# Kernel tuning notes

Measured on AMD Instinct MI355X. Metric: run time of the kernel, lower is better.

The kernel has to match this reference:

```python
import jax, jax.numpy as jnp
import numpy as np

T = 8
TAU = 2.0
V_TH = 1.0
V_RESET = 0.0
ALPHA = 2.0  # ATan surrogate alpha

@jax.custom_vjp
def spike(v):
    # Heaviside(v) with ATan surrogate gradient
    return (v >= 0.0).astype(v.dtype)

def _spike_fwd(v):
    return spike(v), v

def _spike_bwd(v, g):
    sg = (ALPHA / 2.0) / (1.0 + (jnp.pi / 2.0 * ALPHA * v) ** 2)
    return (g * sg,)

spike.defvjp(_spike_fwd, _spike_bwd)

def conv2d(x, w):
    return jax.lax.conv_general_dilated(x, w, (1, 1), 'SAME',
                                        dimension_numbers=('NCHW', 'OIHW', 'NCHW'))

def batchnorm(x, g, b, m, v):
    # inference-mode BN over channel dim of NCHW
    scale = (g / jnp.sqrt(v + 1e-5))[None, :, None, None]
    return (x - m[None, :, None, None]) * scale + b[None, :, None, None]

def maxpool2(x):
    return jax.lax.reduce_window(x, -jnp.inf, jax.lax.max,
                                 (1, 1, 2, 2), (1, 1, 2, 2), 'VALID')

def if_scan(x_seq):
    # x_seq: [T, ...]; IF neuron: v += x; spike; hard reset
    def step(v, x_t):
        v = v + x_t
        s = spike(v - V_TH)
        v = v * (1.0 - s) + V_RESET * s
        return v, s
    v0 = jnp.full_like(x_seq[0], V_RESET)
    _, s_seq = jax.lax.scan(step, v0, x_seq)
    return s_seq

def lif_scan(x_seq):
    # LIF neuron: v += (x - (v - v_reset)) / tau; spike; hard reset
    def step(v, x_t):
        v = v + (x_t - (v - V_RESET)) / TAU
        s = spike(v - V_TH)
        v = v * (1.0 - s) + V_RESET * s
        return v, s
    v0 = jnp.full_like(x_seq[0], V_RESET)
    _, s_seq = jax.lax.scan(step, v0, x_seq)
    return s_seq

def setup_inputs() -> dict:
    key = jax.random.key(0)
    ks = jax.random.split(key, 6)
    B = 64
    d = {
        'x': jax.random.normal(ks[0], (B, 1, 28, 28), dtype=jnp.float32),
        'conv1_w': jax.random.normal(ks[1], (128, 1, 3, 3), dtype=jnp.float32) * 0.3,
        'bn1_g': jnp.ones((128,), jnp.float32),
        'bn1_b': jnp.zeros((128,), jnp.float32),
        'bn1_m': jnp.zeros((128,), jnp.float32),
        'bn1_v': jnp.ones((128,), jnp.float32),
        'conv2_w': jax.random.normal(ks[2], (128, 128, 3, 3), dtype=jnp.float32) * 0.05,
        'bn2_g': jnp.ones((128,), jnp.float32),
        'bn2_b': jnp.zeros((128,), jnp.float32),
        'bn2_m': jnp.zeros((128,), jnp.float32),
        'bn2_v': jnp.ones((128,), jnp.float32),
        'fc1_w': jax.random.normal(ks[3], (128 * 3 * 3, 128 * 7 * 7), dtype=jnp.float32) * 0.02,
        'fc2_w': jax.random.normal(ks[4], (128, 128 * 3 * 3), dtype=jnp.float32) * 0.05,
        'fc3_w': jax.random.normal(ks[5], (10, 128), dtype=jnp.float32) * 0.1,
    }
    return d

def reference(x, conv1_w, bn1_g, bn1_b, bn1_m, bn1_v,
              conv2_w, bn2_g, bn2_b, bn2_m, bn2_v,
              fc1_w, fc2_w, fc3_w):
    B = x.shape[0]
    # static conv + BN (applied once, repeated T times)
    y0 = batchnorm(conv2d(x, conv1_w), bn1_g, bn1_b, bn1_m, bn1_v)  # [B,128,28,28]
    x_seq = jnp.broadcast_to(y0, (T,) + y0.shape)
    s1 = if_scan(x_seq)  # [T,B,128,28,28]
    # pool -> conv -> BN per timestep (vectorized over T*B)
    h = s1.reshape((T * B, 128, 28, 28))
    h = maxpool2(h)                       # [TB,128,14,14]
    h = batchnorm(conv2d(h, conv2_w), bn2_g, bn2_b, bn2_m, bn2_v)
    s2 = if_scan(h.reshape((T, B, 128, 14, 14)))
    # pool -> flatten (dropout is identity in eval mode)
    h = maxpool2(s2.reshape((T * B, 128, 14, 14)))  # [TB,128,7,7]
    h = h.reshape((T, B, 128 * 7 * 7))
    h = jnp.einsum('tbi,oi->tbo', h, fc1_w)   # [T,B,1152]
    s3 = lif_scan(h)
    h = jnp.einsum('tbi,oi->tbo', s3, fc2_w)  # [T,B,128]
    s4 = lif_scan(h)
    h = jnp.einsum('tbi,oi->tbo', s4, fc3_w)  # [T,B,10]
    s5 = lif_scan(h)
    return s5.sum(0) / T
```

## Files before the change

### kernel.cpp

```cpp
#include <hip/hip_runtime.h>
#include <hip/hip_bf16.h>
#include <cstddef>


typedef __attribute__((ext_vector_type(8))) short  short8;
typedef __attribute__((ext_vector_type(4))) float  f32x4;
typedef __attribute__((ext_vector_type(8))) __bf16 bf16x8;

__device__ inline short f2bf_bits(float x) {
    __hip_bfloat16 h = __float2bfloat16(x);
    return *reinterpret_cast<short*>(&h);
}
__device__ inline float bfbits2f(short b) {
    __hip_bfloat16 h;
    *reinterpret_cast<short*>(&h) = b;
    return __bfloat162float(h);
}

__global__ __launch_bounds__(256) void prep2_kernel(
    const float* __restrict__ w2, const float* __restrict__ g2,
    const float* __restrict__ v2, __hip_bfloat16* __restrict__ w2s,
    float* __restrict__ sc2)
{
    int id = blockIdx.x * 256 + threadIdx.x;
    if (id < 128) sc2[id] = g2[id] / sqrtf(v2[id] + 1e-5f);
    int ci = id & 127;
    int co = (id >> 7) & 127;
    int k  = id >> 14;
    float w  = w2[(co * 128 + ci) * 9 + k];
    float hi = __bfloat162float(__float2bfloat16(w));
    float r1 = w - hi;
    float md = __bfloat162float(__float2bfloat16(r1));
    float r2 = r1 - md;
    size_t base = ((size_t)k * 128 + co) * 128 + ci;
    const size_t SPL = 9 * 128 * 128;
    w2s[0 * SPL + base] = __float2bfloat16(hi);
    w2s[1 * SPL + base] = __float2bfloat16(md);
    w2s[2 * SPL + base] = __float2bfloat16(r2);
}

__global__ __launch_bounds__(256) void prep_fc1_kernel(
    const float* __restrict__ w, short* __restrict__ w1s)
{
    int id = blockIdx.x * 256 + threadIdx.x;
    int koct = id % 784;
    int n    = id / 784;
    const float* src = w + (size_t)n * 6272 + koct * 8;
    float4 va = *(const float4*)src;
    float4 vb = *(const float4*)(src + 4);
    float wv[8] = {va.x, va.y, va.z, va.w, vb.x, vb.y, vb.z, vb.w};
    short8 hi8, md8, lo8;
#pragma unroll
    for (int e = 0; e < 8; ++e) {
        float x  = wv[e];
        short hb = f2bf_bits(x);
        float r1 = x - bfbits2f(hb);
        short mb = f2bf_bits(r1);
        float r2 = r1 - bfbits2f(mb);
        hi8[e] = hb; md8[e] = mb; lo8[e] = f2bf_bits(r2);
    }
    const size_t SPL = (size_t)1152 * 6272;
    size_t base = (size_t)n * 6272 + koct * 8;
    *(short8*)&w1s[0 * SPL + base] = hi8;
    *(short8*)&w1s[1 * SPL + base] = md8;
    *(short8*)&w1s[2 * SPL + base] = lo8;
}

__global__ __launch_bounds__(256) void stage1_kernel(
    const float* __restrict__ x,  const float* __restrict__ w1,
    const float* __restrict__ g1, const float* __restrict__ b1,
    const float* __restrict__ m1, const float* __restrict__ v1,
    __hip_bfloat16* __restrict__ p1bf)
{
    int id = blockIdx.x * 256 + threadIdx.x;
    int c  = id & 127;
    int bp = id >> 7;
    int p  = bp % 196;
    int b  = bp / 196;
    int ph = p / 14, pw = p % 14;

    float scale = g1[c] / sqrtf(v1[c] + 1e-5f);
    float mu = m1[c], beta = b1[c];
    float wl[9];
#pragma unroll
    for (int k = 0; k < 9; ++k) wl[k] = w1[c * 9 + k];

    const float* xb = x + b * 784;
    float y[4];
#pragma unroll
    for (int i = 0; i < 4; ++i) {
        int h = 2 * ph + (i >> 1);
        int w = 2 * pw + (i & 1);
        float acc = 0.f;
#pragma unroll
        for (int kh = 0; kh < 3; ++kh) {
#pragma unroll
            for (int kw = 0; kw < 3; ++kw) {
                int hh = h + kh - 1, ww = w + kw - 1;
                if ((unsigned)hh < 28u && (unsigned)ww < 28u)
                    acc += xb[hh * 28 + ww] * wl[kh * 3 + kw];
            }
        }
        y[i] = (acc - mu) * scale + beta;
    }

    float v0 = 0.f, v1m = 0.f, v2m = 0.f, v3m = 0.f;
#pragma unroll
    for (int t = 0; t < 8; ++t) {
        float any = 0.f;
        v0  += y[0]; if (v0  >= 1.0f) { any = 1.0f; v0  = 0.0f; }
        v1m += y[1]; if (v1m >= 1.0f) { any = 1.0f; v1m = 0.0f; }
        v2m += y[2]; if (v2m >= 1.0f) { any = 1.0f; v2m = 0.0f; }
        v3m += y[3]; if (v3m >= 1.0f) { any = 1.0f; v3m = 0.0f; }
        p1bf[((size_t)(t * 64 + b) * 196 + p) * 128 + c] = __float2bfloat16(any);
    }
}

__global__ __launch_bounds__(256, 4) void conv2m_kernel(
    const short* __restrict__ p1bf, const short* __restrict__ w2s,
    const float* __restrict__ sc2,  const float* __restrict__ b2,
    const float* __restrict__ m2,   float* __restrict__ a2t)
{
    __shared__ short patch[272 * 64];
    int bx   = blockIdx.x;
    int tb   = bx >> 1;
    int ch   = bx & 1;
    int tid  = threadIdx.x;
    int lane = tid & 63;
    int wv   = tid >> 6;
    int wm   = wv >> 1, wn = wv & 1;
    int l15  = lane & 15, lg = lane >> 4;

    const short8 z8 = {0, 0, 0, 0, 0, 0, 0, 0};
    for (int idx = tid; idx < 76 * 8; idx += 256) {
        int cell = idx >> 3, q = idx & 7;
        int prow, pcol;
        if (cell < 48) {
            int g = cell >> 4;
            prow = (g == 0) ? 0 : ((g == 1) ? 15 : 16);
            pcol = cell & 15;
        } else {
            int e = cell - 48;
            prow = 1 + (e >> 1);
            pcol = (e & 1) ? 15 : 0;
        }
        *(short8*)&patch[(prow * 16 + pcol) * 64 + q * 8] = z8;
    }

    int abase[7], pbase[7];
#pragma unroll
    for (int mi = 0; mi < 7; ++mi) {
        int pos = (wm * 6 + mi) * 16 + l15;
        int r = pos / 14, c = pos - r * 14;
        abase[mi] = r * 16 + c;
        pbase[mi] = pos;
    }
    int co0 = ch * 64 + wn * 32;

    f32x4 acc[7][2];
#pragma unroll
    for (int mi = 0; mi < 7; ++mi) {
        acc[mi][0] = (f32x4){0.f, 0.f, 0.f, 0.f};
        acc[mi][1] = (f32x4){0.f, 0.f, 0.f, 0.f};
    }

    const short* src = p1bf + (size_t)tb * (196 * 128);
    const size_t SPL = 9 * 128 * 128;

    for (int half = 0; half < 2; ++half) {
        if (half) __syncthreads();
        for (int idx = tid; idx < 196 * 8; idx += 256) {
            int pos = idx >> 3, q = idx & 7;
            short8 v = *(const short8*)&src[pos * 128 + half * 64 + q * 8];
            int h = pos / 14, w = pos - h * 14;
            int lpos = (h + 1) * 16 + (w + 1);
            *(short8*)&patch[lpos * 64 + ((q ^ (pos & 7)) << 3)] = v;
        }
        __syncthreads();

        for (int c2 = 0; c2 < 2; ++c2) {
            int cibase = half * 64 + c2 * 32;
#pragma unroll
            for (int tap = 0; tap < 9; ++tap) {
                const int t16 = (tap / 3) * 16 + (tap % 3);
                const int tc  = (tap / 3 - 1) * 14 + (tap % 3) - 1;
                short8 bfr[3][2];
#pragma unroll
                for (int s = 0; s < 3; ++s)
#pragma unroll
                    for (int nt = 0; nt < 2; ++nt)
                        bfr[s][nt] = *(const short8*)&w2s[s * SPL +
                            ((size_t)tap * 128 + co0 + nt * 16 + l15) * 128 + cibase + lg * 8];
#pragma unroll
                for (int mi = 0; mi < 7; ++mi) {
                    int lpos = abase[mi] + t16;
                    int q2 = (c2 * 4 + lg) ^ ((pbase[mi] + tc) & 7);
                    short8 av = *(const short8*)&patch[lpos * 64 + q2 * 8];
                    if (wm == 1 && mi == 6 && l15 >= 4) av = z8;
                    bf16x8 a = __builtin_bit_cast(bf16x8, av);
#pragma unroll
                    for (int s = 0; s < 3; ++s)
#pragma unroll
                        for (int nt = 0; nt < 2; ++nt)
                            acc[mi][nt] = __builtin_amdgcn_mfma_f32_16x16x32_bf16(
                                a, __builtin_bit_cast(bf16x8, bfr[s][nt]), acc[mi][nt], 0, 0, 0);
                }
            }
        }
    }

    float scv[2], mv[2], bv[2];
#pragma unroll
    for (int nt = 0; nt < 2; ++nt) {
        int co = co0 + nt * 16 + l15;
        scv[nt] = sc2[co]; mv[nt] = m2[co]; bv[nt] = b2[co];
    }
#pragma unroll
    for (int mi = 0; mi < 7; ++mi) {
        int mt = wm * 6 + mi;
#pragma unroll
        for (int nt = 0; nt < 2; ++nt) {
            int co = co0 + nt * 16 + l15;
#pragma unroll
            for (int reg = 0; reg < 4; ++reg) {
                int pos = mt * 16 + lg * 4 + reg;
                if (pos < 196)
                    a2t[((size_t)tb * 196 + pos) * 128 + co] =
                        (acc[mi][nt][reg] - mv[nt]) * scv[nt] + bv[nt];
            }
        }
    }
}

__global__ __launch_bounds__(256) void stage2_kernel(
    const float* __restrict__ a2t, __hip_bfloat16* __restrict__ p2)
{
    int id = blockIdx.x * 256 + threadIdx.x;
    int c  = id & 127;
    int bp = id >> 7;
    int p  = bp % 49;
    int b  = bp / 49;
    int ph = p / 7, pw = p % 7;
    int s0 = (2 * ph) * 14 + 2 * pw;

    float v0 = 0.f, v1 = 0.f, v2 = 0.f, v3 = 0.f;
#pragma unroll
    for (int t = 0; t < 8; ++t) {
        const float* base = a2t + ((size_t)(t * 64 + b) * 196) * 128 + c;
        float x0 = base[(s0) * 128],      x1 = base[(s0 + 1) * 128];
        float x2 = base[(s0 + 14) * 128], x3 = base[(s0 + 15) * 128];
        float any = 0.f;
        v0 += x0; if (v0 >= 1.0f) { any = 1.0f; v0 = 0.0f; }
        v1 += x1; if (v1 >= 1.0f) { any = 1.0f; v1 = 0.0f; }
        v2 += x2; if (v2 >= 1.0f) { any = 1.0f; v2 = 0.0f; }
        v3 += x3; if (v3 >= 1.0f) { any = 1.0f; v3 = 0.0f; }
        p2[(size_t)(t * 64 + b) * 6272 + c * 49 + p] = __float2bfloat16(any);
    }
}

__global__ __launch_bounds__(256, 2) void fc1m_kernel(
    const short* __restrict__ A,
    const short* __restrict__ Bsp,
    float* __restrict__ part)
{
    __shared__ short At[64 * 64];
    const int m0 = blockIdx.x * 64;
    const int n0 = blockIdx.y * 128;
    const int kz = blockIdx.z;
    const int tid  = threadIdx.x;
    const int lane = tid & 63;
    const int wv   = tid >> 6;
    const int wm = wv >> 1, wn = wv & 1;
    const int l15 = lane & 15, lg = lane >> 4;
    const size_t SPL = (size_t)1152 * 6272;

    f32x4 acc[2][4];
#pragma unroll
    for (int mi = 0; mi < 2; ++mi)
#pragma unroll
        for (int nt = 0; nt < 4; ++nt)
            acc[mi][nt] = (f32x4){0.f, 0.f, 0.f, 0.f};

    for (int ks = 0; ks < 14; ++ks) {
        int k0 = kz * 896 + ks * 64;
#pragma unroll
        for (int pp = 0; pp < 2; ++pp) {
            int i = pp * 256 + tid;
            int row = i >> 3, q = i & 7;
            short8 v = *(const short8*)&A[(size_t)(m0 + row) * 6272 + k0 + ((q ^ (row & 7)) << 3)];
            *(short8*)&At[row * 64 + q * 8] = v;
        }
        __syncthreads();

#pragma unroll
        for (int kh = 0; kh < 2; ++kh) {
            bf16x8 a[2];
#pragma unroll
            for (int mi = 0; mi < 2; ++mi) {
                int r = wm * 32 + mi * 16 + l15;
                int q = (kh * 4 + lg) ^ (r & 7);
                a[mi] = __builtin_bit_cast(bf16x8, *(const short8*)&At[r * 64 + q * 8]);
            }
#pragma unroll
            for (int s = 0; s < 3; ++s) {
#pragma unroll
                for (int nt = 0; nt < 4; ++nt) {
                    bf16x8 b = __builtin_bit_cast(bf16x8, *(const short8*)&Bsp[s * SPL +
                        (size_t)(n0 + wn * 64 + nt * 16 + l15) * 6272 + k0 + kh * 32 + lg * 8]);
                    acc[0][nt] = __builtin_amdgcn_mfma_f32_16x16x32_bf16(a[0], b, acc[0][nt], 0, 0, 0);
                    acc[1][nt] = __builtin_amdgcn_mfma_f32_16x16x32_bf16(a[1], b, acc[1][nt], 0, 0, 0);
                }
            }
        }
        __syncthreads();
    }

    float* dst = part + (size_t)kz * (512 * 1152);
#pragma unroll
    for (int mi = 0; mi < 2; ++mi) {
#pragma unroll
        for (int nt = 0; nt < 4; ++nt) {
            int n = n0 + wn * 64 + nt * 16 + l15;
#pragma unroll
            for (int reg = 0; reg < 4; ++reg) {
                int m = m0 + wm * 32 + mi * 16 + lg * 4 + reg;
                dst[(size_t)m * 1152 + n] = acc[mi][nt][reg];
            }
        }
    }
}

__global__ __launch_bounds__(256) void lif2_kernel(
    const float* __restrict__ part, __hip_bfloat16* __restrict__ s3)
{
    int id = blockIdx.x * 256 + threadIdx.x;
    int f = id % 1152;
    int b = id / 1152;
    const size_t S = (size_t)512 * 1152;
    float v = 0.f;
#pragma unroll
    for (int t = 0; t < 8; ++t) {
        size_t off = (size_t)(t * 64 + b) * 1152 + f;
        float x = part[off];
#pragma unroll
        for (int s = 1; s < 7; ++s) x += part[s * S + off];
        v = v + (x - v) * 0.5f;
        s3[off] = __float2bfloat16((v >= 1.0f) ? 1.0f : 0.0f);
        if (v >= 1.0f) v = 0.0f;
    }
}

__global__ __launch_bounds__(256) void fc2tail_kernel(
    const short* __restrict__ s3bf,
    const float* __restrict__ fc2w,
    const float* __restrict__ fc3w,
    float* __restrict__ out)
{
    __shared__ float h2[8][128];
    __shared__ float s4[8][128];
    __shared__ float dd[8][10];
    int b    = blockIdx.x;
    int tid  = threadIdx.x;
    int lane = tid & 63;
    int wv   = tid >> 6;
    int l15  = lane & 15, lg = lane >> 4;

    const short8 z8 = {0, 0, 0, 0, 0, 0, 0, 0};
    f32x4 acc[2] = {(f32x4){0.f, 0.f, 0.f, 0.f}, (f32x4){0.f, 0.f, 0.f, 0.f}};

    for (int ks = 0; ks < 36; ++ks) {
        short8 av = (l15 < 8)
            ? *(const short8*)&s3bf[(size_t)(l15 * 64 + b) * 1152 + ks * 32 + lg * 8]
            : z8;
        bf16x8 a = __builtin_bit_cast(bf16x8, av);
#pragma unroll
        for (int nt = 0; nt < 2; ++nt) {
            int o = wv * 32 + nt * 16 + l15;
            const float* wp = &fc2w[(size_t)o * 1152 + ks * 32 + lg * 8];
            float4 wa = *(const float4*)wp;
            float4 wb = *(const float4*)(wp + 4);
            float wvv[8] = {wa.x, wa.y, wa.z, wa.w, wb.x, wb.y, wb.z, wb.w};
            short8 hi8, md8, lo8;
#pragma unroll
            for (int e = 0; e < 8; ++e) {
                float xw = wvv[e];
                short hb = f2bf_bits(xw);
                float r1 = xw - bfbits2f(hb);
                short mb = f2bf_bits(r1);
                float r2 = r1 - bfbits2f(mb);
                hi8[e] = hb; md8[e] = mb; lo8[e] = f2bf_bits(r2);
            }
            acc[nt] = __builtin_amdgcn_mfma_f32_16x16x32_bf16(
                a, __builtin_bit_cast(bf16x8, hi8), acc[nt], 0, 0, 0);
            acc[nt] = __builtin_amdgcn_mfma_f32_16x16x32_bf16(
                a, __builtin_bit_cast(bf16x8, md8), acc[nt], 0, 0, 0);
            acc[nt] = __builtin_amdgcn_mfma_f32_16x16x32_bf16(
                a, __builtin_bit_cast(bf16x8, lo8), acc[nt], 0, 0, 0);
        }
    }
#pragma unroll
    for (int nt = 0; nt < 2; ++nt) {
#pragma unroll
        for (int reg = 0; reg < 4; ++reg) {
            int t = lg * 4 + reg;
            if (t < 8) h2[t][wv * 32 + nt * 16 + l15] = acc[nt][reg];
        }
    }
    __syncthreads();

    if (tid < 128) {
        float v = 0.f;
#pragma unroll
        for (int t = 0; t < 8; ++t) {
            float xv = h2[t][tid];
            v = v + (xv - v) * 0.5f;
            s4[t][tid] = (v >= 1.0f) ? 1.0f : 0.0f;
            if (v >= 1.0f) v = 0.0f;
        }
    }
    __syncthreads();
    if (tid < 80) {
        int t = tid / 10, o = tid - (tid / 10) * 10;
        float dot = 0.f;
        for (int k = 0; k < 128; ++k) dot += s4[t][k] * fc3w[o * 128 + k];
        dd[t][o] = dot;
    }
    __syncthreads();
    if (tid < 10) {
        float vv = 0.f, cnt = 0.f;
#pragma unroll
        for (int t = 0; t < 8; ++t) {
            float xv = dd[t][tid];
            vv = vv + (xv - vv) * 0.5f;
            if (vv >= 1.0f) { cnt += 1.0f; vv = 0.0f; }
        }
        out[b * 10 + tid] = cnt * 0.125f;
    }
}

extern "C" void kernel_launch(void* const* d_in, const int* in_sizes, int n_in,
                              void* d_out, int out_size, void* d_ws, size_t ws_size,
                              hipStream_t stream)
{
    (void)in_sizes; (void)n_in; (void)out_size; (void)ws_size;
    const float* x    = (const float*)d_in[0];
    const float* w1   = (const float*)d_in[1];
    const float* g1   = (const float*)d_in[2];
    const float* b1   = (const float*)d_in[3];
    const float* m1   = (const float*)d_in[4];
    const float* v1   = (const float*)d_in[5];
    const float* w2   = (const float*)d_in[6];
    const float* g2   = (const float*)d_in[7];
    const float* b2   = (const float*)d_in[8];
    const float* m2   = (const float*)d_in[9];
    const float* v2   = (const float*)d_in[10];
    const float* fc1w = (const float*)d_in[11];
    const float* fc2w = (const float*)d_in[12];
    const float* fc3w = (const float*)d_in[13];
    float* out = (float*)d_out;

    char* ws = (char*)d_ws;
    __hip_bfloat16* p1bf = (__hip_bfloat16*)(ws + 0);
    float*          a2t  = (float*)(ws + 25690112);
    __hip_bfloat16* w2s  = (__hip_bfloat16*)(ws + 77070336);
    float*          sc2  = (float*)(ws + 77955072);
    __hip_bfloat16* p2bf = (__hip_bfloat16*)(ws + 0);
    float*          part = (float*)(ws + 6422528);
    __hip_bfloat16* s3bf = (__hip_bfloat16*)(ws + 22937600);
    short*          w1s  = (short*)(ws + 25690112);

    prep2_kernel   <<<576,  256, 0, stream>>>(w2, g2, v2, w2s, sc2);
    stage1_kernel  <<<6272, 256, 0, stream>>>(x, w1, g1, b1, m1, v1, p1bf);
    conv2m_kernel  <<<1024, 256, 0, stream>>>((const short*)p1bf, (const short*)w2s,
                                              sc2, b2, m2, a2t);
    stage2_kernel  <<<1568, 256, 0, stream>>>(a2t, p2bf);
    prep_fc1_kernel<<<3528, 256, 0, stream>>>(fc1w, w1s);
    fc1m_kernel    <<<dim3(8, 9, 7), 256, 0, stream>>>((const short*)p2bf, w1s, part);
    lif2_kernel    <<<288,  256, 0, stream>>>(part, s3bf);
    fc2tail_kernel <<<64,   256, 0, stream>>>((const short*)s3bf, fc2w, fc3w, out);
}
```

Baseline: 439.1 us.

## Stage full 128-channel patch once and prefetch conv2 weight fragments

The conv2 MFMA kernel now loads all 128 input channels of the pooled spike patch into shared memory in one pass, doubling LDS use and removing the mid-kernel barrier between channel halves. Weight fragments for the next tap are software-prefetched into registers while the current tap's MFMAs run, hiding global load latency. Block-to-work mapping is changed so the two output-channel halves of the same timestep-batch are far apart in the grid, and launch bounds drop to 2 blocks per SM. The larger LDS footprint and extra live registers reduce occupancy in exchange for fewer syncs and better latency hiding.

```diff
diff --git a/kernel.cpp b/kernel.cpp
--- a/kernel.cpp
+++ b/kernel.cpp
@@ -116,15 +116,15 @@
     }
 }
 
-__global__ __launch_bounds__(256, 4) void conv2m_kernel(
+__global__ __launch_bounds__(256, 2) void conv2m_kernel(
     const short* __restrict__ p1bf, const short* __restrict__ w2s,
     const float* __restrict__ sc2,  const float* __restrict__ b2,
     const float* __restrict__ m2,   float* __restrict__ a2t)
 {
-    __shared__ short patch[272 * 64];
+    __shared__ short patch[272 * 128];
     int bx   = blockIdx.x;
-    int tb   = bx >> 1;
-    int ch   = bx & 1;
+    int tb   = bx & 511;
+    int ch   = bx >> 9;
     int tid  = threadIdx.x;
     int lane = tid & 63;
     int wv   = tid >> 6;
@@ -132,8 +132,8 @@
     int l15  = lane & 15, lg = lane >> 4;
 
     const short8 z8 = {0, 0, 0, 0, 0, 0, 0, 0};
-    for (int idx = tid; idx < 76 * 8; idx += 256) {
-        int cell = idx >> 3, q = idx & 7;
+    for (int idx = tid; idx < 76 * 16; idx += 256) {
+        int cell = idx >> 4, sl = idx & 15;
         int prow, pcol;
         if (cell < 48) {
             int g = cell >> 4;
@@ -144,8 +144,17 @@
             prow = 1 + (e >> 1);
             pcol = (e & 1) ? 15 : 0;
         }
-        *(short8*)&patch[(prow * 16 + pcol) * 64 + q * 8] = z8;
-    }
+        *(short8*)&patch[(prow * 16 + pcol) * 128 + sl * 8] = z8;
+    }
+    const short* src = p1bf + (size_t)tb * (196 * 128);
+    for (int idx = tid; idx < 196 * 16; idx += 256) {
+        int pos = idx >> 4, q = idx & 15;
+        short8 v = *(const short8*)&src[pos * 128 + q * 8];
+        int h = pos / 14, w = pos - h * 14;
+        int lpos = (h + 1) * 16 + (w + 1);
+        *(short8*)&patch[lpos * 128 + ((q ^ (pos & 7)) << 3)] = v;
+    }
+    __syncthreads();
 
     int abase[7], pbase[7];
 #pragma unroll
@@ -164,48 +173,50 @@
         acc[mi][1] = (f32x4){0.f, 0.f, 0.f, 0.f};
     }
 
-    const short* src = p1bf + (size_t)tb * (196 * 128);
     const size_t SPL = 9 * 128 * 128;
-
-    for (int half = 0; half < 2; ++half) {
-        if (half) __syncthreads();
-        for (int idx = tid; idx < 196 * 8; idx += 256) {
-            int pos = idx >> 3, q = idx & 7;
-            short8 v = *(const short8*)&src[pos * 128 + half * 64 + q * 8];
-            int h = pos / 14, w = pos - h * 14;
-            int lpos = (h + 1) * 16 + (w + 1);
-            *(short8*)&patch[lpos * 64 + ((q ^ (pos & 7)) << 3)] = v;
-        }
-        __syncthreads();
-
-        for (int c2 = 0; c2 < 2; ++c2) {
-            int cibase = half * 64 + c2 * 32;
-#pragma unroll
-            for (int tap = 0; tap < 9; ++tap) {
-                const int t16 = (tap / 3) * 16 + (tap % 3);
-                const int tc  = (tap / 3 - 1) * 14 + (tap % 3) - 1;
-                short8 bfr[3][2];
+    short8 bcur[3][2];
+#pragma unroll
+    for (int s = 0; s < 3; ++s)
+#pragma unroll
+        for (int nt = 0; nt < 2; ++nt)
+            bcur[s][nt] = *(const short8*)&w2s[s * SPL +
+                ((size_t)0 * 128 + co0 + nt * 16 + l15) * 128 + 0 * 32 + lg * 8];
+
+#pragma unroll 1
+    for (int chunk = 0; chunk < 4; ++chunk) {
+#pragma unroll
+        for (int tap = 0; tap < 9; ++tap) {
+            int ntap   = (tap == 8) ? 0 : tap + 1;
+            int nchunk = (tap == 8) ? ((chunk < 3) ? chunk + 1 : 3) : chunk;
+            short8 bnxt[3][2];
+#pragma unroll
+            for (int s = 0; s < 3; ++s)
+#pragma unroll
+                for (int nt = 0; nt < 2; ++nt)
+                    bnxt[s][nt] = *(const short8*)&w2s[s * SPL +
+                        ((size_t)ntap * 128 + co0 + nt * 16 + l15) * 128 + nchunk * 32 + lg * 8];
+
+            const int t16 = (tap / 3) * 16 + (tap % 3);
+            const int tc  = (tap / 3 - 1) * 14 + (tap % 3) - 1;
+#pragma unroll
+            for (int mi = 0; mi < 7; ++mi) {
+                int lpos = abase[mi] + t16;
+                int q2 = (chunk * 4 + lg) ^ ((pbase[mi] + tc) & 7);
+                short8 av = *(const short8*)&patch[lpos * 128 + q2 * 8];
+                if (wm == 1 && mi == 6 && l15 >= 4) av = z8;
+                bf16x8 a = __builtin_bit_cast(bf16x8, av);
 #pragma unroll
                 for (int s = 0; s < 3; ++s)
 #pragma unroll
                     for (int nt = 0; nt < 2; ++nt)
-                        bfr[s][nt] = *(const short8*)&w2s[s * SPL +
-                            ((size_t)tap * 128 + co0 + nt * 16 + l15) * 128 + cibase + lg * 8];
-#pragma unroll
-                for (int mi = 0; mi < 7; ++mi) {
-                    int lpos = abase[mi] + t16;
-                    int q2 = (c2 * 4 + lg) ^ ((pbase[mi] + tc) & 7);
-                    short8 av = *(const short8*)&patch[lpos * 64 + q2 * 8];
-                    if (wm == 1 && mi == 6 && l15 >= 4) av = z8;
-                    bf16x8 a = __builtin_bit_cast(bf16x8, av);
-#pragma unroll
-                    for (int s = 0; s < 3; ++s)
-#pragma unroll
-                        for (int nt = 0; nt < 2; ++nt)
-                            acc[mi][nt] = __builtin_amdgcn_mfma_f32_16x16x32_bf16(
-                                a, __builtin_bit_cast(bf16x8, bfr[s][nt]), acc[mi][nt], 0, 0, 0);
-                }
-            }
+                        acc[mi][nt] = __builtin_amdgcn_mfma_f32_16x16x32_bf16(
+                            a, __builtin_bit_cast(bf16x8, bcur[s][nt]), acc[mi][nt], 0, 0, 0);
+            }
+#pragma unroll
+            for (int s = 0; s < 3; ++s)
+#pragma unroll
+                for (int nt = 0; nt < 2; ++nt)
+                    bcur[s][nt] = bnxt[s][nt];
         }
     }
 
```

Measured after the change: 430.6 us. No clear change (-1.9%).
